# Performance work log

Hardware: AMD Instinct MI355X
Metric: run time of the kernel (lower is better)

## Reference

```python
import jax, jax.numpy as jnp
import numpy as np

WID = 61
SIGMA = 1.0
PAD = WID // 2  # 30, reflect padding so conv output matches input H,W


def _gauss_kernel():
    # Matches ContentLoss.make_gauss_kernel: block-diagonal == depthwise.
    ks = min(max(3, WID), 150)
    mean = np.floor(0.5 * ks)
    x = np.arange(ks, dtype=np.float64)
    k1 = np.exp(-(x - mean) ** 2 / (2.0 * SIGMA ** 2))
    k2 = np.outer(k1, k1).astype(np.float32)
    k2 = k2 / np.sum(k2)
    # depthwise kernel [C_out=3, C_in/groups=1, kh, kw]
    return jnp.asarray(np.tile(k2[None, None], (3, 1, 1, 1)))


def _avg_g(x, k):
    xp = jnp.pad(x, ((0, 0), (0, 0), (PAD, PAD), (PAD, PAD)), mode='reflect')
    return jax.lax.conv_general_dilated(
        xp, k, window_strides=(1, 1), padding='VALID',
        dimension_numbers=('NCHW', 'OIHW', 'NCHW'),
        feature_group_count=3)


def setup_inputs() -> dict:
    key = jax.random.key(0)
    ka, kb = jax.random.split(key)
    a = jax.random.normal(ka, (16, 3, 512, 512), dtype=jnp.float32)
    b = jax.random.normal(kb, (16, 3, 512, 512), dtype=jnp.float32)
    return {"a": a, "b": b}


def reference(a, b):
    k = _gauss_kernel()
    ga = _avg_g(a, k).mean(axis=1)  # [B, H, W]
    gb = _avg_g(b, k).mean(axis=1)
    d = ga - gb
    return (d * d).mean()
```

## Files before the change

### kernel.cpp

```cpp
#include <hip/hip_runtime.h>
#include <math.h>


#define R 6
#define HW 512
#define NB 16
#define NPIX (16.0f * 512.0f * 512.0f)

struct GaussW { float w[R + 1]; };

__global__ __launch_bounds__(128) void cl_pass1(
    const float* __restrict__ A, const float* __restrict__ B,
    float* __restrict__ T, GaussW gw) {
  const int row  = blockIdx.x;
  const int bimg = row >> 9;
  const int y    = row & (HW - 1);
  const int tid  = threadIdx.x;
  const int x    = tid << 2;

  __shared__ float e[HW + 2 * R];

  const size_t base = ((size_t)bimg * 3 * HW + y) * HW;
  float4 s = {0.f, 0.f, 0.f, 0.f};
#pragma unroll
  for (int c = 0; c < 3; ++c) {
    const float4 av = *reinterpret_cast<const float4*>(A + base + (size_t)c * HW * HW + x);
    const float4 bv = *reinterpret_cast<const float4*>(B + base + (size_t)c * HW * HW + x);
    s.x += av.x - bv.x;
    s.y += av.y - bv.y;
    s.z += av.z - bv.z;
    s.w += av.w - bv.w;
  }
  const float inv3 = 1.0f / 3.0f;
  e[R + x + 0] = s.x * inv3;
  e[R + x + 1] = s.y * inv3;
  e[R + x + 2] = s.z * inv3;
  e[R + x + 3] = s.w * inv3;
  __syncthreads();
  if (tid < R) {
    e[R - 1 - tid]    = e[R + 1 + tid];
    e[R + HW + tid]   = e[R + HW - 2 - tid];
  }
  __syncthreads();

  float4 o;
  float* op = &o.x;
#pragma unroll
  for (int k = 0; k < 4; ++k) {
    const int xi = R + x + k;
    float acc = gw.w[0] * e[xi];
#pragma unroll
    for (int d = 1; d <= R; ++d) acc += gw.w[d] * (e[xi - d] + e[xi + d]);
    op[k] = acc;
  }
  *reinterpret_cast<float4*>(T + (size_t)row * HW + x) = o;
}

__global__ __launch_bounds__(256) void cl_pass2(
    const float* __restrict__ T, float* __restrict__ out, GaussW gw) {
  const int bid  = blockIdx.x;
  const int bimg = bid >> 5;
  const int rem  = bid & 31;
  const int xs   = rem & 1;
  const int yc   = rem >> 1;
  const int x    = (xs << 8) + threadIdx.x;
  const int y0   = yc << 5;

  const float* tb = T + (size_t)bimg * HW * HW;

  float acc = 0.f;
#pragma unroll 4
  for (int yy = 0; yy < 32; ++yy) {
    const int y = y0 + yy;
    float v = gw.w[0] * tb[(size_t)y * HW + x];
#pragma unroll
    for (int d = 1; d <= R; ++d) {
      int ym = y - d; ym = (ym < 0) ? -ym : ym;
      int yp = y + d; yp = (yp > HW - 1) ? (2 * (HW - 1) - yp) : yp;
      v += gw.w[d] * (tb[(size_t)ym * HW + x] + tb[(size_t)yp * HW + x]);
    }
    acc += v * v;
  }

#pragma unroll
  for (int off = 32; off > 0; off >>= 1) acc += __shfl_down(acc, off, 64);
  __shared__ float wsum[4];
  const int lane = threadIdx.x & 63;
  const int wv   = threadIdx.x >> 6;
  if (lane == 0) wsum[wv] = acc;
  __syncthreads();
  if (threadIdx.x == 0) {
    const float s = wsum[0] + wsum[1] + wsum[2] + wsum[3];
    atomicAdd(out, s * (1.0f / NPIX));
  }
}

extern "C" void kernel_launch(void* const* d_in, const int* in_sizes, int n_in,
                              void* d_out, int out_size, void* d_ws, size_t ws_size,
                              hipStream_t stream) {
  const float* A = (const float*)d_in[0];
  const float* B = (const float*)d_in[1];
  float* out = (float*)d_out;
  float* T = (float*)d_ws;

  GaussW gw;
  {
    double S = 0.0;
    for (int i = 0; i < 61; ++i) {
      const double dd = (double)i - 30.0;
      S += exp(-dd * dd * 0.5);
    }
    for (int d = 0; d <= R; ++d)
      gw.w[d] = (float)(exp(-(double)(d * d) * 0.5) / S);
  }

  hipMemsetAsync(d_out, 0, sizeof(float), stream);
  cl_pass1<<<NB * HW, 128, 0, stream>>>(A, B, T, gw);
  cl_pass2<<<NB * 32, 256, 0, stream>>>(T, out, gw);
}
```

Before: 128.3 us.

## Use wave-per-row horizontal blur with shuffles, nontemporal loads, drop memset

Pass 1 now assigns one 64-lane wave per image row, with each lane handling 8 pixels. The horizontal halo and reflect padding are exchanged through lane shuffles instead of shared memory and two block barriers. Input loads use nontemporal hints, and zeroing the output moves from a separate hipMemsetAsync into pass 1, which removes one launch. Each lane now holds more registers, and the output zeroing relies on pass 1 finishing before pass 2 starts on the same stream.

Measured after the change: 136.2 us. 6.1% more time.

```diff
diff --git a/kernel.cpp b/kernel.cpp
--- a/kernel.cpp
+++ b/kernel.cpp
@@ -4,56 +4,74 @@
 
 #define R 6
 #define HW 512
-#define NB 16
+#define CS (HW * HW)
 #define NPIX (16.0f * 512.0f * 512.0f)
+
+typedef float f4 __attribute__((ext_vector_type(4)));
 
 struct GaussW { float w[R + 1]; };
 
-__global__ __launch_bounds__(128) void cl_pass1(
+__global__ __launch_bounds__(256) void cl_pass1(
     const float* __restrict__ A, const float* __restrict__ B,
-    float* __restrict__ T, GaussW gw) {
-  const int row  = blockIdx.x;
+    float* __restrict__ T, float* __restrict__ out, GaussW gw) {
+  const int tid  = threadIdx.x;
+  const int lane = tid & 63;
+  const int row  = (blockIdx.x << 2) + (tid >> 6);
   const int bimg = row >> 9;
   const int y    = row & (HW - 1);
-  const int tid  = threadIdx.x;
-  const int x    = tid << 2;
+  const int x    = lane << 3;
 
-  __shared__ float e[HW + 2 * R];
+  if (row == 0 && lane == 0) *out = 0.f;
 
-  const size_t base = ((size_t)bimg * 3 * HW + y) * HW;
-  float4 s = {0.f, 0.f, 0.f, 0.f};
+  const size_t base = ((size_t)bimg * 3 * HW + y) * HW + (size_t)x;
+  const float* pa = A + base;
+  const float* pb = B + base;
+
+  f4 a00 = __builtin_nontemporal_load((const f4*)(pa));
+  f4 a01 = __builtin_nontemporal_load((const f4*)(pa + 4));
+  f4 a10 = __builtin_nontemporal_load((const f4*)(pa + CS));
+  f4 a11 = __builtin_nontemporal_load((const f4*)(pa + CS + 4));
+  f4 a20 = __builtin_nontemporal_load((const f4*)(pa + 2 * CS));
+  f4 a21 = __builtin_nontemporal_load((const f4*)(pa + 2 * CS + 4));
+  f4 b00 = __builtin_nontemporal_load((const f4*)(pb));
+  f4 b01 = __builtin_nontemporal_load((const f4*)(pb + 4));
+  f4 b10 = __builtin_nontemporal_load((const f4*)(pb + CS));
+  f4 b11 = __builtin_nontemporal_load((const f4*)(pb + CS + 4));
+  f4 b20 = __builtin_nontemporal_load((const f4*)(pb + 2 * CS));
+  f4 b21 = __builtin_nontemporal_load((const f4*)(pb + 2 * CS + 4));
+
+  const float inv3 = 1.0f / 3.0f;
+  f4 s0 = ((a00 - b00) + (a10 - b10) + (a20 - b20)) * inv3;
+  f4 s1 = ((a01 - b01) + (a11 - b11) + (a21 - b21)) * inv3;
+
+  float ev[8] = {s0.x, s0.y, s0.z, s0.w, s1.x, s1.y, s1.z, s1.w};
+
+  float ew[20];
 #pragma unroll
-  for (int c = 0; c < 3; ++c) {
-    const float4 av = *reinterpret_cast<const float4*>(A + base + (size_t)c * HW * HW + x);
-    const float4 bv = *reinterpret_cast<const float4*>(B + base + (size_t)c * HW * HW + x);
-    s.x += av.x - bv.x;
-    s.y += av.y - bv.y;
-    s.z += av.z - bv.z;
-    s.w += av.w - bv.w;
+  for (int j = 0; j < 8; ++j) ew[6 + j] = ev[j];
+#pragma unroll
+  for (int d = 1; d <= R; ++d) {
+    const float v = __shfl_up(ev[8 - d], 1, 64);
+    ew[6 - d] = (lane == 0) ? ev[d] : v;
   }
-  const float inv3 = 1.0f / 3.0f;
-  e[R + x + 0] = s.x * inv3;
-  e[R + x + 1] = s.y * inv3;
-  e[R + x + 2] = s.z * inv3;
-  e[R + x + 3] = s.w * inv3;
-  __syncthreads();
-  if (tid < R) {
-    e[R - 1 - tid]    = e[R + 1 + tid];
-    e[R + HW + tid]   = e[R + HW - 2 - tid];
+#pragma unroll
+  for (int t = 0; t < R; ++t) {
+    const float u = __shfl_down(ev[t], 1, 64);
+    ew[14 + t] = (lane == 63) ? ev[6 - t] : u;
   }
-  __syncthreads();
 
-  float4 o;
-  float* op = &o.x;
+  float o[8];
 #pragma unroll
-  for (int k = 0; k < 4; ++k) {
-    const int xi = R + x + k;
-    float acc = gw.w[0] * e[xi];
+  for (int k = 0; k < 8; ++k) {
+    float acc = gw.w[0] * ew[6 + k];
 #pragma unroll
-    for (int d = 1; d <= R; ++d) acc += gw.w[d] * (e[xi - d] + e[xi + d]);
-    op[k] = acc;
+    for (int d = 1; d <= R; ++d) acc += gw.w[d] * (ew[6 + k - d] + ew[6 + k + d]);
+    o[k] = acc;
   }
-  *reinterpret_cast<float4*>(T + (size_t)row * HW + x) = o;
+
+  float* tp = T + (size_t)row * HW + x;
+  *reinterpret_cast<f4*>(tp)     = (f4){o[0], o[1], o[2], o[3]};
+  *reinterpret_cast<f4*>(tp + 4) = (f4){o[4], o[5], o[6], o[7]};
 }
 
 __global__ __launch_bounds__(256) void cl_pass2(
@@ -114,7 +132,6 @@
       gw.w[d] = (float)(exp(-(double)(d * d) * 0.5) / S);
   }
 
-  hipMemsetAsync(d_out, 0, sizeof(float), stream);
-  cl_pass1<<<NB * HW, 128, 0, stream>>>(A, B, T, gw);
-  cl_pass2<<<NB * 32, 256, 0, stream>>>(T, out, gw);
+  cl_pass1<<<(16 * HW) / 4, 256, 0, stream>>>(A, B, T, out, gw);
+  cl_pass2<<<16 * 32, 256, 0, stream>>>(T, out, gw);
 }
```
